# Optimization experiments

Hardware: AMD Instinct MI355X
Metric: run time of the kernel (lower is better)

## Reference

```python
import jax, jax.numpy as jnp
import numpy as np
import math

# Module hyperparameters (match init_kwargs)
T_FRAMES = 12
LEN_Q = 8160          # sum_l H_l*W_l for levels (64,96),(32,48),(16,24),(8,12)
D_MODEL = 256
N_HEADS = 8
N_LEVELS = 4
T_WINDOW = 2
N_CURR = 4            # n_curr_points
N_TEMP = 2            # n_temporal_points
D_HEAD = D_MODEL // N_HEADS


def _offset_biases():
    """Replicates _reset_parameters() grid init for the offset biases."""
    thetas = np.arange(N_HEADS, dtype=np.float32) * (2.0 * math.pi / N_HEADS)
    grid = np.stack([np.cos(thetas), np.sin(thetas)], -1)            # (H, 2)
    grid = grid / np.abs(grid).max(-1, keepdims=True)
    curr = np.tile(grid.reshape(N_HEADS, 1, 1, 2), (1, N_LEVELS, N_CURR, 1))
    curr = curr * (np.arange(1, N_CURR + 1, dtype=np.float32).reshape(1, 1, N_CURR, 1))
    temp = np.tile(grid.reshape(N_HEADS, 1, 1, 1, 2), (1, N_LEVELS, T_WINDOW, N_TEMP, 1))
    temp = temp * (np.arange(1, N_TEMP + 1, dtype=np.float32).reshape(1, 1, 1, N_TEMP, 1))
    return jnp.asarray(curr.reshape(-1)), jnp.asarray(temp.reshape(-1))


def setup_inputs() -> dict:
    key = jax.random.key(0)
    ks = jax.random.split(key, 10)
    s = 0.02
    b_so, b_tso = _offset_biases()
    d_so = N_HEADS * N_LEVELS * N_CURR * 2          # 256
    d_aw = N_HEADS * N_LEVELS * N_CURR              # 128
    d_tso = N_HEADS * N_LEVELS * T_WINDOW * N_TEMP * 2  # 512
    d_taw = N_HEADS * N_LEVELS * T_WINDOW * N_TEMP      # 256
    return {
        "query": jax.random.normal(ks[0], (T_FRAMES, LEN_Q, D_MODEL), jnp.float32),
        "input_flatten": jax.random.normal(ks[1], (T_FRAMES, LEN_Q, D_MODEL), jnp.float32),
        "W_val": jax.random.normal(ks[2], (D_MODEL, D_MODEL), jnp.float32) * s,
        "b_val": jnp.zeros((D_MODEL,), jnp.float32),
        "W_so": jax.random.normal(ks[3], (D_MODEL, d_so), jnp.float32) * s,
        "b_so": b_so,
        "W_aw": jax.random.normal(ks[4], (D_MODEL, d_aw), jnp.float32) * s,
        "b_aw": jnp.zeros((d_aw,), jnp.float32),
        "W_tso": jax.random.normal(ks[5], (D_MODEL, d_tso), jnp.float32) * s,
        "b_tso": b_tso,
        "W_taw": jax.random.normal(ks[6], (D_MODEL, d_taw), jnp.float32) * s,
        "b_taw": jnp.zeros((d_taw,), jnp.float32),
    }


def reference(query, input_flatten, W_val, b_val, W_so, b_so, W_aw, b_aw,
              W_tso, b_tso, W_taw, b_taw):
    T, Lq, _ = query.shape
    # value projection -> (T, Len_in, H, D_head)
    value = (input_flatten @ W_val + b_val).reshape(T, -1, N_HEADS, D_HEAD)
    # current-frame sampling offsets -> (T, Lq, H, L, n_curr, 2)
    curr_off = (query @ W_so + b_so).reshape(T, Lq, N_HEADS, N_LEVELS, N_CURR, 2)
    # temporal sampling offsets -> (T, Lq, H, t_window*L, n_temp, 2) (flatten(3,4))
    temp_off = (query @ W_tso + b_tso).reshape(
        T, Lq, N_HEADS, T_WINDOW, N_LEVELS, N_TEMP, 2
    ).reshape(T, Lq, N_HEADS, T_WINDOW * N_LEVELS, N_TEMP, 2)
    # joint softmax over current + temporal attention logits
    caw = (query @ W_aw + b_aw).reshape(T, Lq, N_HEADS, N_LEVELS * N_CURR)
    taw = (query @ W_taw + b_taw).reshape(T, Lq, N_HEADS, T_WINDOW * N_LEVELS * N_TEMP)
    aw = jax.nn.softmax(jnp.concatenate([caw, taw], axis=-1), axis=-1)
    n_c = N_LEVELS * N_CURR
    aw_curr = aw[..., :n_c].reshape(T, Lq, N_HEADS, N_LEVELS, N_CURR)
    aw_temp = aw[..., n_c:].reshape(T, Lq, N_HEADS, T_WINDOW * N_LEVELS, N_TEMP)
    return (value, curr_off, temp_off, aw_curr, aw_temp)
```

## Files before the change

kernel.cpp:

```cpp
#include <hip/hip_runtime.h>
#include <hip/hip_bf16.h>
#include <stdint.h>

#define AS1 __attribute__((address_space(1)))
#define AS3 __attribute__((address_space(3)))

typedef __attribute__((ext_vector_type(8))) short short8;
typedef __attribute__((ext_vector_type(4))) float floatx4;

__device__ __forceinline__ unsigned short f2b_rne(float f) {
  union { float f; unsigned u; } c; c.f = f;
  unsigned u = c.u;
  unsigned r = u + 0x7fffu + ((u >> 16) & 1u);
  return (unsigned short)(r >> 16);
}

__global__ void prep_weights(const float* __restrict__ Wv,  const float* __restrict__ bv,
                             const float* __restrict__ Wso, const float* __restrict__ bso,
                             const float* __restrict__ Waw, const float* __restrict__ baw,
                             const float* __restrict__ Wtso,const float* __restrict__ btso,
                             const float* __restrict__ Wtaw,const float* __restrict__ btaw,
                             unsigned short* __restrict__ Wt, float* __restrict__ bcat) {
  int n = blockIdx.x;
  int k = threadIdx.x;
  const float* W; const float* b; int c, N;
  if (n < 256)      { W = Wv;   b = bv;   c = n;       N = 256; }
  else if (n < 512) { W = Wso;  b = bso;  c = n - 256; N = 256; }
  else if (n < 768) { W = Wtso; b = btso; c = n - 512; N = 256; }
  else if (n < 896) { W = Waw;  b = baw;  c = n - 768; N = 128; }
  else              { W = Wtaw; b = btaw; c = n - 896; N = 128; }
  Wt[n * 256 + k] = f2b_rne(W[(size_t)k * N + c]);
  if (k == 0) bcat[n] = b[c];
}

__global__ __launch_bounds__(256, 3)
void gemm_main(const float* __restrict__ Q, const float* __restrict__ X,
               const unsigned short* __restrict__ Wt, const float* __restrict__ bcat,
               float* __restrict__ out, int M) {
  __shared__ __align__(16) unsigned short As[128 * 32];
  __shared__ __align__(16) unsigned short Bs[128 * 32];

  const int nt = blockIdx.x;
  const int mt = blockIdx.y;
  const int mBase = mt * 128;
  const int nBase = nt * 128;
  const float* A = (nt < 2) ? X : Q;

  const int tid  = threadIdx.x;
  const int lane = tid & 63;
  const int wid  = tid >> 6;
  const int mw   = (wid >> 1) * 64;
  const int nw   = (wid & 1) * 64;
  const int lrow = lane & 15;
  const int quad = lane >> 4;

  floatx4 acc[4][4] = {};

  const float* Ab = A + (size_t)mBase * 256;
  const unsigned short* Bb = Wt + (size_t)nBase * 256;

  for (int s = 0; s < 8; ++s) {
    const int k0 = s * 32;
    __syncthreads();
#pragma unroll
    for (int j = 0; j < 2; ++j) {
      int ch = j * 256 + tid;
      int r = ch >> 2, kc = ch & 3;
      const unsigned short* g = Bb + (size_t)r * 256 + k0 + kc * 8;
      unsigned ldsoff = (unsigned)((j * 256 + (tid & ~63)) * 16);
      __builtin_amdgcn_global_load_lds((const AS1 void*)g,
                                       (AS3 void*)(((char*)Bs) + ldsoff), 16, 0, 0);
    }
    float4 va[4];
#pragma unroll
    for (int i = 0; i < 4; ++i) {
      int id = i * 256 + tid;
      int r = id >> 3, kc = id & 7;
      va[i] = *(const float4*)(Ab + (size_t)r * 256 + k0 + kc * 4);
    }
#pragma unroll
    for (int i = 0; i < 4; ++i) {
      int id = i * 256 + tid;
      uint2 pk;
      pk.x = ((unsigned)f2b_rne(va[i].y) << 16) | f2b_rne(va[i].x);
      pk.y = ((unsigned)f2b_rne(va[i].w) << 16) | f2b_rne(va[i].z);
      *(uint2*)(&As[id * 4]) = pk;
    }
    __syncthreads();
    short8 af[4], bf[4];
#pragma unroll
    for (int mi = 0; mi < 4; ++mi)
      af[mi] = *(const short8*)(&As[(mw + mi * 16 + lrow) * 32 + quad * 8]);
#pragma unroll
    for (int ni = 0; ni < 4; ++ni)
      bf[ni] = *(const short8*)(&Bs[(nw + ni * 16 + lrow) * 32 + quad * 8]);
#pragma unroll
    for (int mi = 0; mi < 4; ++mi)
#pragma unroll
      for (int ni = 0; ni < 4; ++ni)
        acc[mi][ni] = __builtin_amdgcn_mfma_f32_16x16x32_bf16(af[mi], bf[ni], acc[mi][ni], 0, 0, 0);
  }

  const int seg  = nt >> 1;
  const int half = nt & 1;
  float* Oseg = out + (size_t)seg * ((size_t)M * 256) + (size_t)half * 128;
#pragma unroll
  for (int ni = 0; ni < 4; ++ni) {
    float bias = bcat[nBase + nw + ni * 16 + lrow];
#pragma unroll
    for (int mi = 0; mi < 4; ++mi) {
#pragma unroll
      for (int r = 0; r < 4; ++r) {
        int row = mBase + mw + mi * 16 + quad * 4 + r;
        int col = nw + ni * 16 + lrow;
        Oseg[(size_t)row * 256 + col] = acc[mi][ni][r] + bias;
      }
    }
  }
}

__global__ __launch_bounds__(256, 2)
void gemm_aw(const float* __restrict__ Q, const unsigned short* __restrict__ Wt,
             const float* __restrict__ bcat, float* __restrict__ awc,
             float* __restrict__ awt, int M) {
  __shared__ __align__(16) float Ls[64 * 256];
  unsigned short* As = (unsigned short*)Ls;
  unsigned short* Bs = ((unsigned short*)Ls) + 2048;

  const int mt = blockIdx.x;
  const int mBase = mt * 64;

  const int tid  = threadIdx.x;
  const int lane = tid & 63;
  const int wid  = tid >> 6;
  const int nw   = wid * 64;
  const int lrow = lane & 15;
  const int quad = lane >> 4;

  floatx4 acc[4][4] = {};

  const float* Ab = Q + (size_t)mBase * 256;
  const unsigned short* Bb = Wt + (size_t)768 * 256;

  for (int s = 0; s < 8; ++s) {
    const int k0 = s * 32;
    __syncthreads();
#pragma unroll
    for (int j = 0; j < 4; ++j) {
      int ch = j * 256 + tid;
      int r = ch >> 2, kc = ch & 3;
      const unsigned short* g = Bb + (size_t)r * 256 + k0 + kc * 8;
      unsigned ldsoff = 4096u + (unsigned)((j * 256 + (tid & ~63)) * 16);
      __builtin_amdgcn_global_load_lds((const AS1 void*)g,
                                       (AS3 void*)(((char*)Ls) + ldsoff), 16, 0, 0);
    }
    float4 va[2];
#pragma unroll
    for (int i = 0; i < 2; ++i) {
      int id = i * 256 + tid;
      int r = id >> 3, kc = id & 7;
      va[i] = *(const float4*)(Ab + (size_t)r * 256 + k0 + kc * 4);
    }
#pragma unroll
    for (int i = 0; i < 2; ++i) {
      int id = i * 256 + tid;
      uint2 pk;
      pk.x = ((unsigned)f2b_rne(va[i].y) << 16) | f2b_rne(va[i].x);
      pk.y = ((unsigned)f2b_rne(va[i].w) << 16) | f2b_rne(va[i].z);
      *(uint2*)(&As[id * 4]) = pk;
    }
    __syncthreads();
    short8 af[4], bf[4];
#pragma unroll
    for (int mi = 0; mi < 4; ++mi)
      af[mi] = *(const short8*)(&As[(mi * 16 + lrow) * 32 + quad * 8]);
#pragma unroll
    for (int ni = 0; ni < 4; ++ni)
      bf[ni] = *(const short8*)(&Bs[(nw + ni * 16 + lrow) * 32 + quad * 8]);
#pragma unroll
    for (int mi = 0; mi < 4; ++mi)
#pragma unroll
      for (int ni = 0; ni < 4; ++ni)
        acc[mi][ni] = __builtin_amdgcn_mfma_f32_16x16x32_bf16(af[mi], bf[ni], acc[mi][ni], 0, 0, 0);
  }

  __syncthreads();

#pragma unroll
  for (int ni = 0; ni < 4; ++ni) {
    float bias = bcat[768 + nw + ni * 16 + lrow];
#pragma unroll
    for (int mi = 0; mi < 4; ++mi) {
#pragma unroll
      for (int r = 0; r < 4; ++r) {
        int row = mi * 16 + quad * 4 + r;
        int col = nw + ni * 16 + lrow;
        Ls[row * 256 + col] = acc[mi][ni][r] + bias;
      }
    }
  }
  __syncthreads();

#pragma unroll
  for (int i = 0; i < 2; ++i) {
    int p = i * 256 + tid;
    int row = p >> 3, h = p & 7;
    const float* lc = &Ls[row * 256 + h * 16];
    const float* lt = &Ls[row * 256 + 128 + h * 16];
    float v[32];
#pragma unroll
    for (int j = 0; j < 16; ++j) { v[j] = lc[j]; v[16 + j] = lt[j]; }
    float mx = v[0];
#pragma unroll
    for (int j = 1; j < 32; ++j) mx = fmaxf(mx, v[j]);
    float ssum = 0.f;
#pragma unroll
    for (int j = 0; j < 32; ++j) { v[j] = __expf(v[j] - mx); ssum += v[j]; }
    float inv = 1.0f / ssum;
    float* oc = awc + (size_t)(mBase + row) * 128 + h * 16;
    float* ot = awt + (size_t)(mBase + row) * 128 + h * 16;
#pragma unroll
    for (int g = 0; g < 4; ++g) {
      float4 c4 = make_float4(v[g*4+0]*inv, v[g*4+1]*inv, v[g*4+2]*inv, v[g*4+3]*inv);
      float4 t4 = make_float4(v[16+g*4+0]*inv, v[16+g*4+1]*inv, v[16+g*4+2]*inv, v[16+g*4+3]*inv);
      *(float4*)(oc + g * 4) = c4;
      *(float4*)(ot + g * 4) = t4;
    }
  }
}

extern "C" void kernel_launch(void* const* d_in, const int* in_sizes, int n_in,
                              void* d_out, int out_size, void* d_ws, size_t ws_size,
                              hipStream_t stream) {
  const float* Q    = (const float*)d_in[0];
  const float* Xf   = (const float*)d_in[1];
  const float* Wv   = (const float*)d_in[2];
  const float* bv   = (const float*)d_in[3];
  const float* Wso  = (const float*)d_in[4];
  const float* bso  = (const float*)d_in[5];
  const float* Waw  = (const float*)d_in[6];
  const float* baw  = (const float*)d_in[7];
  const float* Wtso = (const float*)d_in[8];
  const float* btso = (const float*)d_in[9];
  const float* Wtaw = (const float*)d_in[10];
  const float* btaw = (const float*)d_in[11];
  float* out = (float*)d_out;

  unsigned short* Wt = (unsigned short*)d_ws;
  float* bcat = (float*)((char*)d_ws + 1024 * 256 * 2);

  int M = in_sizes[0] / 256;

  prep_weights<<<1024, 256, 0, stream>>>(Wv, bv, Wso, bso, Waw, baw,
                                         Wtso, btso, Wtaw, btaw, Wt, bcat);

  dim3 g1(6, M / 128);
  gemm_main<<<g1, 256, 0, stream>>>(Q, Xf, Wt, bcat, out, M);

  float* awc = out + (size_t)3 * M * 256;
  float* awt = awc + (size_t)M * 128;
  gemm_aw<<<M / 64, 256, 0, stream>>>(Q, Wt, bcat, awc, awt, M);
}
```

Measured before the change: 213.2 us.

## Fuse all projection GEMMs and softmax into one row-tile kernel with swizzled LDS

Replaces the two GEMM kernels with one kernel per 64-row tile. Each tile converts its whole X slab, then its whole Q slab, to bf16 in LDS once and loops over all output column tiles, so Q is read from global memory once instead of five times. The attention-weight GEMM is computed in transposed form so the joint softmax can be done in registers with lane shuffles instead of going through LDS. It adds XOR swizzles to the weight layout and the LDS layout to avoid bank conflicts, and writes the outputs as float4. In exchange, the grid becomes a single 1D launch of fewer, longer blocks, with more serial work per block and larger LDS use that may lower occupancy.

```diff
diff --git a/kernel.cpp b/kernel.cpp
--- a/kernel.cpp
+++ b/kernel.cpp
@@ -1,5 +1,4 @@
 #include <hip/hip_runtime.h>
-#include <hip/hip_bf16.h>
 #include <stdint.h>
 
 #define AS1 __attribute__((address_space(1)))
@@ -29,202 +28,185 @@
   else if (n < 768) { W = Wtso; b = btso; c = n - 512; N = 256; }
   else if (n < 896) { W = Waw;  b = baw;  c = n - 768; N = 128; }
   else              { W = Wtaw; b = btaw; c = n - 896; N = 128; }
-  Wt[n * 256 + k] = f2b_rne(W[(size_t)k * N + c]);
+  int c8 = k >> 3, lo = k & 7;
+  int cs;
+  if (n < 768) cs = (c8 & ~7) | ((c8 ^ n) & 7);
+  else         cs = (c8 & ~3) | ((c8 ^ n) & 3);
+  Wt[n * 256 + cs * 8 + lo] = f2b_rne(W[(size_t)k * N + c]);
   if (k == 0) bcat[n] = b[c];
 }
 
 __global__ __launch_bounds__(256, 3)
-void gemm_main(const float* __restrict__ Q, const float* __restrict__ X,
+void fused_all(const float* __restrict__ Q, const float* __restrict__ X,
                const unsigned short* __restrict__ Wt, const float* __restrict__ bcat,
                float* __restrict__ out, int M) {
-  __shared__ __align__(16) unsigned short As[128 * 32];
-  __shared__ __align__(16) unsigned short Bs[128 * 32];
-
-  const int nt = blockIdx.x;
-  const int mt = blockIdx.y;
-  const int mBase = mt * 128;
-  const int nBase = nt * 128;
-  const float* A = (nt < 2) ? X : Q;
+  __shared__ __align__(16) char lds[49152];
 
   const int tid  = threadIdx.x;
   const int lane = tid & 63;
   const int wid  = tid >> 6;
-  const int mw   = (wid >> 1) * 64;
-  const int nw   = (wid & 1) * 64;
   const int lrow = lane & 15;
   const int quad = lane >> 4;
-
-  floatx4 acc[4][4] = {};
-
-  const float* Ab = A + (size_t)mBase * 256;
-  const unsigned short* Bb = Wt + (size_t)nBase * 256;
-
+  const int mw   = (wid >> 1) * 32;
+  const int nw   = (wid & 1) * 64;
+  const int mBase = blockIdx.x * 64;
+
+  for (int phase = 0; phase < 2; ++phase) {
+    const float* A = (phase == 0) ? X : Q;
+    {
+      float4 va[16];
+#pragma unroll
+      for (int i = 0; i < 16; ++i) {
+        int id = i * 256 + tid;
+        int r = id >> 6, c4 = id & 63;
+        va[i] = *(const float4*)(A + (size_t)(mBase + r) * 256 + c4 * 4);
+      }
+#pragma unroll
+      for (int i = 0; i < 16; ++i) {
+        int id = i * 256 + tid;
+        int r = id >> 6, c4 = id & 63;
+        int c8 = c4 >> 1, hf = c4 & 1;
+        int pos = (c8 & ~7) | ((c8 ^ r) & 7);
+        uint2 pk;
+        pk.x = ((unsigned)f2b_rne(va[i].y) << 16) | f2b_rne(va[i].x);
+        pk.y = ((unsigned)f2b_rne(va[i].w) << 16) | f2b_rne(va[i].z);
+        *(uint2*)(lds + r * 512 + pos * 16 + hf * 8) = pk;
+      }
+    }
+    const int ntBeg = phase ? 2 : 0;
+    const int ntEnd = phase ? 6 : 2;
+    for (int nt = ntBeg; nt < ntEnd; ++nt) {
+      const int nBase = nt * 128;
+      const unsigned short* Bb = Wt + (size_t)nBase * 256;
+      floatx4 acc[2][4] = {};
+      for (int s = 0; s < 4; ++s) {
+#pragma unroll
+        for (int ci = 0; ci < 4; ++ci) {
+          int g = ci * 256 + tid;
+          int r = g >> 3, j = g & 7;
+          const unsigned short* src = Bb + (size_t)r * 256 + s * 64 + j * 8;
+          unsigned ldsoff = 32768u + (unsigned)((ci * 256 + (tid & ~63)) * 16);
+          __builtin_amdgcn_global_load_lds((const AS1 void*)src,
+                                           (AS3 void*)(lds + ldsoff), 16, 0, 0);
+        }
+        __syncthreads();
+        short8 af[2][2], bf[4][2];
+#pragma unroll
+        for (int mi = 0; mi < 2; ++mi) {
+          int row = mw + mi * 16 + lrow;
+#pragma unroll
+          for (int kk = 0; kk < 2; ++kk) {
+            int j = kk * 4 + quad;
+            af[mi][kk] = *(const short8*)(lds + row * 512 + (s * 8 + (j ^ (row & 7))) * 16);
+          }
+        }
+#pragma unroll
+        for (int ni = 0; ni < 4; ++ni) {
+          int r = nw + ni * 16 + lrow;
+#pragma unroll
+          for (int kk = 0; kk < 2; ++kk) {
+            int j = kk * 4 + quad;
+            bf[ni][kk] = *(const short8*)(lds + 32768 + r * 128 + ((j ^ (r & 7)) * 16));
+          }
+        }
+#pragma unroll
+        for (int kk = 0; kk < 2; ++kk)
+#pragma unroll
+          for (int mi = 0; mi < 2; ++mi)
+#pragma unroll
+            for (int ni = 0; ni < 4; ++ni)
+              acc[mi][ni] = __builtin_amdgcn_mfma_f32_16x16x32_bf16(
+                  bf[ni][kk], af[mi][kk], acc[mi][ni], 0, 0, 0);
+        __syncthreads();
+      }
+      const int seg = nt >> 1, halfn = nt & 1;
+      float* O = out + (size_t)seg * ((size_t)M * 256) + halfn * 128;
+#pragma unroll
+      for (int ni = 0; ni < 4; ++ni) {
+        float4 b4 = *(const float4*)(bcat + nBase + nw + ni * 16 + quad * 4);
+#pragma unroll
+        for (int mi = 0; mi < 2; ++mi) {
+          int row = mBase + mw + mi * 16 + lrow;
+          float4 v;
+          v.x = acc[mi][ni][0] + b4.x;
+          v.y = acc[mi][ni][1] + b4.y;
+          v.z = acc[mi][ni][2] + b4.z;
+          v.w = acc[mi][ni][3] + b4.w;
+          *(float4*)(O + (size_t)row * 256 + nw + ni * 16 + quad * 4) = v;
+        }
+      }
+    }
+  }
+
+  floatx4 acc2[4][4] = {};
   for (int s = 0; s < 8; ++s) {
-    const int k0 = s * 32;
+#pragma unroll
+    for (int ci = 0; ci < 4; ++ci) {
+      int g = ci * 64 + lane;
+      int sr = g >> 2, j = g & 3;
+      int n = (sr < 32) ? (768 + 32 * wid + sr) : (896 + 32 * wid + (sr - 32));
+      const unsigned short* src = Wt + (size_t)n * 256 + s * 32 + j * 8;
+      unsigned ldsoff = 32768u + (unsigned)(wid * 4096 + ci * 1024);
+      __builtin_amdgcn_global_load_lds((const AS1 void*)src,
+                                       (AS3 void*)(lds + ldsoff), 16, 0, 0);
+    }
     __syncthreads();
-#pragma unroll
-    for (int j = 0; j < 2; ++j) {
-      int ch = j * 256 + tid;
-      int r = ch >> 2, kc = ch & 3;
-      const unsigned short* g = Bb + (size_t)r * 256 + k0 + kc * 8;
-      unsigned ldsoff = (unsigned)((j * 256 + (tid & ~63)) * 16);
-      __builtin_amdgcn_global_load_lds((const AS1 void*)g,
-                                       (AS3 void*)(((char*)Bs) + ldsoff), 16, 0, 0);
-    }
-    float4 va[4];
-#pragma unroll
-    for (int i = 0; i < 4; ++i) {
-      int id = i * 256 + tid;
-      int r = id >> 3, kc = id & 7;
-      va[i] = *(const float4*)(Ab + (size_t)r * 256 + k0 + kc * 4);
-    }
-#pragma unroll
-    for (int i = 0; i < 4; ++i) {
-      int id = i * 256 + tid;
-      uint2 pk;
-      pk.x = ((unsigned)f2b_rne(va[i].y) << 16) | f2b_rne(va[i].x);
-      pk.y = ((unsigned)f2b_rne(va[i].w) << 16) | f2b_rne(va[i].z);
-      *(uint2*)(&As[id * 4]) = pk;
-    }
+    short8 wa[4], qf[4];
+#pragma unroll
+    for (int t = 0; t < 4; ++t) {
+      wa[t] = *(const short8*)(lds + 32768 + wid * 4096 + (t * 16 + lrow) * 64 +
+                               (quad ^ (lrow & 3)) * 16);
+    }
+#pragma unroll
+    for (int qt = 0; qt < 4; ++qt) {
+      int row = qt * 16 + lrow;
+      int cg = s * 4 + quad;
+      int pos = (cg & ~7) | ((cg ^ (row & 7)) & 7);
+      qf[qt] = *(const short8*)(lds + row * 512 + pos * 16);
+    }
+#pragma unroll
+    for (int qt = 0; qt < 4; ++qt)
+#pragma unroll
+      for (int t = 0; t < 4; ++t)
+        acc2[qt][t] = __builtin_amdgcn_mfma_f32_16x16x32_bf16(
+            wa[t], qf[qt], acc2[qt][t], 0, 0, 0);
     __syncthreads();
-    short8 af[4], bf[4];
-#pragma unroll
-    for (int mi = 0; mi < 4; ++mi)
-      af[mi] = *(const short8*)(&As[(mw + mi * 16 + lrow) * 32 + quad * 8]);
-#pragma unroll
-    for (int ni = 0; ni < 4; ++ni)
-      bf[ni] = *(const short8*)(&Bs[(nw + ni * 16 + lrow) * 32 + quad * 8]);
-#pragma unroll
-    for (int mi = 0; mi < 4; ++mi)
-#pragma unroll
-      for (int ni = 0; ni < 4; ++ni)
-        acc[mi][ni] = __builtin_amdgcn_mfma_f32_16x16x32_bf16(af[mi], bf[ni], acc[mi][ni], 0, 0, 0);
   }
 
-  const int seg  = nt >> 1;
-  const int half = nt & 1;
-  float* Oseg = out + (size_t)seg * ((size_t)M * 256) + (size_t)half * 128;
-#pragma unroll
-  for (int ni = 0; ni < 4; ++ni) {
-    float bias = bcat[nBase + nw + ni * 16 + lrow];
-#pragma unroll
-    for (int mi = 0; mi < 4; ++mi) {
-#pragma unroll
-      for (int r = 0; r < 4; ++r) {
-        int row = mBase + mw + mi * 16 + quad * 4 + r;
-        int col = nw + ni * 16 + lrow;
-        Oseg[(size_t)row * 256 + col] = acc[mi][ni][r] + bias;
-      }
-    }
-  }
-}
-
-__global__ __launch_bounds__(256, 2)
-void gemm_aw(const float* __restrict__ Q, const unsigned short* __restrict__ Wt,
-             const float* __restrict__ bcat, float* __restrict__ awc,
-             float* __restrict__ awt, int M) {
-  __shared__ __align__(16) float Ls[64 * 256];
-  unsigned short* As = (unsigned short*)Ls;
-  unsigned short* Bs = ((unsigned short*)Ls) + 2048;
-
-  const int mt = blockIdx.x;
-  const int mBase = mt * 64;
-
-  const int tid  = threadIdx.x;
-  const int lane = tid & 63;
-  const int wid  = tid >> 6;
-  const int nw   = wid * 64;
-  const int lrow = lane & 15;
-  const int quad = lane >> 4;
-
-  floatx4 acc[4][4] = {};
-
-  const float* Ab = Q + (size_t)mBase * 256;
-  const unsigned short* Bb = Wt + (size_t)768 * 256;
-
-  for (int s = 0; s < 8; ++s) {
-    const int k0 = s * 32;
-    __syncthreads();
-#pragma unroll
-    for (int j = 0; j < 4; ++j) {
-      int ch = j * 256 + tid;
-      int r = ch >> 2, kc = ch & 3;
-      const unsigned short* g = Bb + (size_t)r * 256 + k0 + kc * 8;
-      unsigned ldsoff = 4096u + (unsigned)((j * 256 + (tid & ~63)) * 16);
-      __builtin_amdgcn_global_load_lds((const AS1 void*)g,
-                                       (AS3 void*)(((char*)Ls) + ldsoff), 16, 0, 0);
-    }
-    float4 va[2];
-#pragma unroll
-    for (int i = 0; i < 2; ++i) {
-      int id = i * 256 + tid;
-      int r = id >> 3, kc = id & 7;
-      va[i] = *(const float4*)(Ab + (size_t)r * 256 + k0 + kc * 4);
-    }
-#pragma unroll
-    for (int i = 0; i < 2; ++i) {
-      int id = i * 256 + tid;
-      uint2 pk;
-      pk.x = ((unsigned)f2b_rne(va[i].y) << 16) | f2b_rne(va[i].x);
-      pk.y = ((unsigned)f2b_rne(va[i].w) << 16) | f2b_rne(va[i].z);
-      *(uint2*)(&As[id * 4]) = pk;
-    }
-    __syncthreads();
-    short8 af[4], bf[4];
-#pragma unroll
-    for (int mi = 0; mi < 4; ++mi)
-      af[mi] = *(const short8*)(&As[(mi * 16 + lrow) * 32 + quad * 8]);
-#pragma unroll
-    for (int ni = 0; ni < 4; ++ni)
-      bf[ni] = *(const short8*)(&Bs[(nw + ni * 16 + lrow) * 32 + quad * 8]);
-#pragma unroll
-    for (int mi = 0; mi < 4; ++mi)
-#pragma unroll
-      for (int ni = 0; ni < 4; ++ni)
-        acc[mi][ni] = __builtin_amdgcn_mfma_f32_16x16x32_bf16(af[mi], bf[ni], acc[mi][ni], 0, 0, 0);
-  }
-
-  __syncthreads();
-
-#pragma unroll
-  for (int ni = 0; ni < 4; ++ni) {
-    float bias = bcat[768 + nw + ni * 16 + lrow];
-#pragma unroll
-    for (int mi = 0; mi < 4; ++mi) {
-#pragma unroll
-      for (int r = 0; r < 4; ++r) {
-        int row = mi * 16 + quad * 4 + r;
-        int col = nw + ni * 16 + lrow;
-        Ls[row * 256 + col] = acc[mi][ni][r] + bias;
-      }
-    }
-  }
-  __syncthreads();
-
-#pragma unroll
-  for (int i = 0; i < 2; ++i) {
-    int p = i * 256 + tid;
-    int row = p >> 3, h = p & 7;
-    const float* lc = &Ls[row * 256 + h * 16];
-    const float* lt = &Ls[row * 256 + 128 + h * 16];
-    float v[32];
-#pragma unroll
-    for (int j = 0; j < 16; ++j) { v[j] = lc[j]; v[16 + j] = lt[j]; }
-    float mx = v[0];
-#pragma unroll
-    for (int j = 1; j < 32; ++j) mx = fmaxf(mx, v[j]);
-    float ssum = 0.f;
-#pragma unroll
-    for (int j = 0; j < 32; ++j) { v[j] = __expf(v[j] - mx); ssum += v[j]; }
-    float inv = 1.0f / ssum;
-    float* oc = awc + (size_t)(mBase + row) * 128 + h * 16;
-    float* ot = awt + (size_t)(mBase + row) * 128 + h * 16;
-#pragma unroll
-    for (int g = 0; g < 4; ++g) {
-      float4 c4 = make_float4(v[g*4+0]*inv, v[g*4+1]*inv, v[g*4+2]*inv, v[g*4+3]*inv);
-      float4 t4 = make_float4(v[16+g*4+0]*inv, v[16+g*4+1]*inv, v[16+g*4+2]*inv, v[16+g*4+3]*inv);
-      *(float4*)(oc + g * 4) = c4;
-      *(float4*)(ot + g * 4) = t4;
+  float* awc = out + (size_t)3 * ((size_t)M * 256);
+  float* awt = awc + (size_t)M * 128;
+#pragma unroll
+  for (int hp = 0; hp < 2; ++hp) {
+    const int h = 2 * wid + hp;
+    float4 bc = *(const float4*)(bcat + 768 + h * 16 + quad * 4);
+    float4 bt = *(const float4*)(bcat + 896 + h * 16 + quad * 4);
+#pragma unroll
+    for (int qt = 0; qt < 4; ++qt) {
+      float c0 = acc2[qt][hp][0] + bc.x;
+      float c1 = acc2[qt][hp][1] + bc.y;
+      float c2 = acc2[qt][hp][2] + bc.z;
+      float c3 = acc2[qt][hp][3] + bc.w;
+      float t0 = acc2[qt][2 + hp][0] + bt.x;
+      float t1 = acc2[qt][2 + hp][1] + bt.y;
+      float t2 = acc2[qt][2 + hp][2] + bt.z;
+      float t3 = acc2[qt][2 + hp][3] + bt.w;
+      float mx = fmaxf(fmaxf(fmaxf(c0, c1), fmaxf(c2, c3)),
+                       fmaxf(fmaxf(t0, t1), fmaxf(t2, t3)));
+      mx = fmaxf(mx, __shfl_xor(mx, 16));
+      mx = fmaxf(mx, __shfl_xor(mx, 32));
+      float e0 = __expf(c0 - mx), e1 = __expf(c1 - mx);
+      float e2 = __expf(c2 - mx), e3 = __expf(c3 - mx);
+      float f0 = __expf(t0 - mx), f1 = __expf(t1 - mx);
+      float f2 = __expf(t2 - mx), f3 = __expf(t3 - mx);
+      float sm = ((e0 + e1) + (e2 + e3)) + ((f0 + f1) + (f2 + f3));
+      sm += __shfl_xor(sm, 16);
+      sm += __shfl_xor(sm, 32);
+      float inv = 1.0f / sm;
+      int row = mBase + qt * 16 + lrow;
+      float4 oc = make_float4(e0 * inv, e1 * inv, e2 * inv, e3 * inv);
+      float4 ot = make_float4(f0 * inv, f1 * inv, f2 * inv, f3 * inv);
+      *(float4*)(awc + (size_t)row * 128 + h * 16 + quad * 4) = oc;
+      *(float4*)(awt + (size_t)row * 128 + h * 16 + quad * 4) = ot;
     }
   }
 }
@@ -254,10 +236,5 @@
   prep_weights<<<1024, 256, 0, stream>>>(Wv, bv, Wso, bso, Waw, baw,
                                          Wtso, btso, Wtaw, btaw, Wt, bcat);
 
-  dim3 g1(6, M / 128);
-  gemm_main<<<g1, 256, 0, stream>>>(Q, Xf, Wt, bcat, out, M);
-
-  float* awc = out + (size_t)3 * M * 256;
-  float* awt = awc + (size_t)M * 128;
-  gemm_aw<<<M / 64, 256, 0, stream>>>(Q, Wt, bcat, awc, awt, M);
-}
+  fused_all<<<M / 64, 256, 0, stream>>>(Q, Xf, Wt, bcat, out, M);
+}
```

Measured after the change: 187.2 us. 12.2% less time.
